# Kernel tuning notes

Measured on AMD Instinct MI355X. Metric: run time of the kernel, lower is better.

## Reference

```python
import jax, jax.numpy as jnp
import numpy as np

# ---- static config (from grid_conf / data_aug_conf) ----
B, N, C = 4, 6, 64            # batch, cameras, camC
OGH, OGW = 256, 704           # final_dim
DOWN = 16                     # 32 // up_scale
FH, FW = OGH // DOWN, OGW // DOWN   # 16, 44
DB0, DB1, DBS = 4.0, 45.0, 1.0      # dbound
D = int((DB1 - DB0) / DBS)          # 41 depth bins
DX = np.array([0.5, 0.5, 20.0], np.float32)            # dx
BX = np.array([-49.75, -49.75, 0.0], np.float32)        # bx (lower + dx/2)
NX = (200, 200, 1)                                       # nx


def make_frustum():
    # [D, FH, FW, 3] pixel (u, v, depth) frustum, matches torch create_frustum
    ds = jnp.arange(DB0, DB1, DBS, dtype=jnp.float32)[:, None, None] * jnp.ones((1, FH, FW), jnp.float32)
    xs = jnp.linspace(0.0, OGW - 1.0, FW, dtype=jnp.float32)[None, None, :] * jnp.ones((D, FH, 1), jnp.float32)
    ys = jnp.linspace(0.0, OGH - 1.0, FH, dtype=jnp.float32)[None, :, None] * jnp.ones((D, 1, FW), jnp.float32)
    return jnp.stack([xs, ys, ds], axis=-1)


def get_geometry(rots, trans, intrins, post_rots, post_trans):
    # frustum points -> ego frame, [B, N, D, FH, FW, 3]
    pts = make_frustum()[None, None] - post_trans[:, :, None, None, None, :]
    pts = jnp.einsum('bnij,bndhwj->bndhwi', jnp.linalg.inv(post_rots), pts)
    # un-project: (u*d, v*d, d)
    pts = jnp.concatenate([pts[..., :2] * pts[..., 2:3], pts[..., 2:3]], axis=-1)
    combine = rots @ jnp.linalg.inv(intrins)
    return jnp.einsum('bnij,bndhwj->bndhwi', combine, pts) + trans[:, :, None, None, None, :]


def voxel_pooling(geom, x):
    # geom: [B,N,D,H,W,3] ego coords; x: [B,N,D,H,W,C] lifted features
    dx = jnp.asarray(DX); bx = jnp.asarray(BX)
    # voxel indices; .astype(int32) truncates toward zero like torch .long()
    gi = ((geom - (bx - dx / 2.0)) / dx).astype(jnp.int32)
    Np = B * N * D * FH * FW
    gi = gi.reshape(Np, 3)
    xf = x.reshape(Np, C)
    bidx = jnp.repeat(jnp.arange(B, dtype=jnp.int32), N * D * FH * FW)
    valid = ((gi[:, 0] >= 0) & (gi[:, 0] < NX[0]) &
             (gi[:, 1] >= 0) & (gi[:, 1] < NX[1]) &
             (gi[:, 2] >= 0) & (gi[:, 2] < NX[2]))
    # flat voxel id: (((b*nz + z)*nx0 + xi)*nx1 + yi)
    flat = ((bidx * NX[2] + gi[:, 2]) * NX[0] + gi[:, 0]) * NX[1] + gi[:, 1]
    flat = jnp.where(valid, flat, 0)
    xf = xf * valid[:, None].astype(xf.dtype)
    nvox = B * NX[2] * NX[0] * NX[1]
    # scatter-add == sort + cumsum-trick per-voxel sum in the torch code
    final = jax.ops.segment_sum(xf, flat, num_segments=nvox)          # [nvox, C]
    final = final.reshape(B, NX[2], NX[0], NX[1], C)
    final = jnp.transpose(final, (0, 1, 4, 2, 3)).reshape(B, NX[2] * C, NX[0], NX[1])
    return final


def setup_inputs() -> dict:
    key = jax.random.key(0)
    k1, k2 = jax.random.split(key)
    feat_depth = jax.random.normal(k1, (B, N, D, FH, FW), jnp.float32)
    feat_pv = jax.random.normal(k2, (B, N, C, FH, FW), jnp.float32)
    # realistic 6-camera nuScenes-like rig, intrinsics scaled to 704x256
    base = np.array([[0., 0., 1.], [-1., 0., 0.], [0., -1., 0.]], np.float32)  # cam axes -> ego axes
    rots = np.zeros((B, N, 3, 3), np.float32)
    trans = np.zeros((B, N, 3), np.float32)
    for n in range(N):
        yaw = 2.0 * np.pi * n / N
        Rz = np.array([[np.cos(yaw), -np.sin(yaw), 0.], [np.sin(yaw), np.cos(yaw), 0.], [0., 0., 1.]], np.float32)
        rots[:, n] = Rz @ base
        trans[:, n] = Rz @ np.array([1.5, 0.0, 1.6], np.float32)
    fx = 1266.0 * (OGW / 1600.0)
    intr = np.array([[fx, 0., OGW / 2.0], [0., fx, OGH / 2.0], [0., 0., 1.]], np.float32)
    return {
        'feat_depth': feat_depth,
        'feat_pv': feat_pv,
        'rots': jnp.asarray(rots),
        'trans': jnp.asarray(trans),
        'intrins': jnp.asarray(np.broadcast_to(intr, (B, N, 3, 3)).copy()),
        'post_rots': jnp.asarray(np.broadcast_to(np.eye(3, dtype=np.float32), (B, N, 3, 3)).copy()),
        'post_trans': jnp.zeros((B, N, 3), jnp.float32),
    }


def reference(feat_depth, feat_pv, rots, trans, intrins, post_rots, post_trans):
    geom = get_geometry(rots, trans, intrins, post_rots, post_trans)
    geom = jax.lax.stop_gradient(geom)  # torch casts to .long(): indices are non-diff
    depth = jax.nn.softmax(feat_depth, axis=2)                 # get_depth_dist over D
    # lift: depth.unsqueeze(1) * feat.unsqueeze(2) -> [B,N,D,C,H,W] -> [B,N,D,H,W,C]
    x = depth[:, :, :, None] * feat_pv[:, :, None]
    x = jnp.transpose(x, (0, 1, 2, 4, 5, 3))
    return voxel_pooling(geom, x)                               # [B, C*nz, 200, 200]
```

## Files before the change

### kernel.cpp

```cpp
#include <hip/hip_runtime.h>
#include <math.h>

namespace {
constexpr int kB = 4, kN = 6, kC = 64, kD = 41, kFH = 16, kFW = 44;
constexpr int kNX0 = 200, kNX1 = 200;
constexpr int kHW  = kFH * kFW;
constexpr int kPix = kB * kN * kHW;
constexpr int kPts = kPix * kD;
constexpr int kVox = kB * kNX0 * kNX1;
constexpr int kPvElems = kPix * kC;
constexpr int kScanBlks = kVox / 256;
constexpr int kPvtTiles = kPix / 64;

constexpr size_t kOffPvT    = 0;
constexpr size_t kSzPvT     = (size_t)kPvElems * 4;
constexpr size_t kOffVox    = kOffPvT + kSzPvT;
constexpr size_t kSzVox     = (size_t)kPts * 4;
constexpr size_t kOffWgt    = kOffVox + kSzVox;
constexpr size_t kSzWgt     = (size_t)kPts * 4;
constexpr size_t kOffCnt    = kOffWgt + kSzWgt;
constexpr size_t kSzCnt     = (size_t)kVox * 4;
constexpr size_t kOffOffs   = kOffCnt + kSzCnt;
constexpr size_t kSzOffs    = 640256;
constexpr size_t kOffBSum   = kOffOffs + kSzOffs;
constexpr size_t kSzBSum    = 2560;
constexpr size_t kOffSKW    = kOffBSum + kSzBSum;
constexpr size_t kSzSKW     = (size_t)kPts * 8;
constexpr size_t kWsNeed    = kOffSKW + kSzSKW + 256;
}

__device__ __forceinline__ void inv3x3(const float m[9], float inv[9]) {
    float a = m[0], b = m[1], c = m[2];
    float d = m[3], e = m[4], f = m[5];
    float g = m[6], h = m[7], i = m[8];
    float A =  (e * i - f * h);
    float Bm = -(d * i - f * g);
    float Cm =  (d * h - e * g);
    float det = a * A + b * Bm + c * Cm;
    float r = 1.0f / det;
    inv[0] = A * r;
    inv[1] = -(b * i - c * h) * r;
    inv[2] =  (b * f - c * e) * r;
    inv[3] = Bm * r;
    inv[4] =  (a * i - c * g) * r;
    inv[5] = -(a * f - c * d) * r;
    inv[6] = Cm * r;
    inv[7] = -(a * h - b * g) * r;
    inv[8] =  (a * e - b * d) * r;
}

__global__ __launch_bounds__(256) void lss_pvt(const float* __restrict__ pv,
                                               float* __restrict__ pvT,
                                               unsigned* __restrict__ counts) {
    __shared__ float t[64][65];
    const int blk = blockIdx.x;
    const int tid = threadIdx.x;
    const int ci = blk * 256 + tid;
    if (ci < kVox) counts[ci] = 0u;

    if (blk < kPvtTiles) {
        const int pix0 = blk * 64;
        const int bn  = pix0 / kHW;
        const int hw0 = pix0 - bn * kHW;
        const int lane = tid & 63;
        const int wv   = tid >> 6;
        const float* src = pv + (size_t)(bn * kC) * kHW + hw0;
#pragma unroll
        for (int cc = 0; cc < 16; ++cc) {
            const int c = wv * 16 + cc;
            t[c][lane] = src[(size_t)c * kHW + lane];
        }
        __syncthreads();
        float* dst = pvT + (size_t)pix0 * kC;
#pragma unroll
        for (int jj = 0; jj < 16; ++jj) {
            const int j = wv * 16 + jj;
            dst[j * kC + lane] = t[lane][j];
        }
    }
}

__global__ __launch_bounds__(256) void lss_sm(const float* __restrict__ feat_depth,
                                              float* __restrict__ wgtArr) {
    const int pix = blockIdx.x * 256 + threadIdx.x;
    const int bn = pix / kHW;
    const int hw = pix - bn * kHW;
    const float* p = feat_depth + (size_t)(bn * kD) * kHW + hw;
    float v[kD];
#pragma unroll
    for (int d = 0; d < kD; ++d) v[d] = p[(size_t)d * kHW];
    float mx = v[0];
#pragma unroll
    for (int d = 1; d < kD; ++d) mx = fmaxf(mx, v[d]);
    float sm = 0.0f;
#pragma unroll
    for (int d = 0; d < kD; ++d) { v[d] = __expf(v[d] - mx); sm += v[d]; }
    const float inv = 1.0f / sm;
    float* o = wgtArr + (size_t)(bn * kD) * kHW + hw;
#pragma unroll
    for (int d = 0; d < kD; ++d) o[(size_t)d * kHW] = v[d] * inv;
}

__global__ __launch_bounds__(256) void lss_geo(
    const float* __restrict__ rots,
    const float* __restrict__ trans,
    const float* __restrict__ intrins,
    const float* __restrict__ post_rots,
    const float* __restrict__ post_trans,
    int* __restrict__ voxArr,
    unsigned* __restrict__ counts)
{
    const int q   = blockIdx.x * 256 + threadIdx.x;
    const int bn  = q / (kD * kHW);
    const int rem = q - bn * (kD * kHW);
    const int d   = rem / kHW;
    const int hw  = rem - d * kHW;
    const int h   = hw / kFW;
    const int w   = hw - h * kFW;
    const int b   = bn / kN;

    const float* R  = rots       + bn * 9;
    const float* K  = intrins    + bn * 9;
    const float* PR = post_rots  + bn * 9;
    const float* PT = post_trans + bn * 3;
    const float* T  = trans      + bn * 3;

    float Km[9], PRm[9];
#pragma unroll
    for (int i = 0; i < 9; ++i) { Km[i] = K[i]; PRm[i] = PR[i]; }
    float invK[9], invPR[9];
    inv3x3(Km, invK);
    inv3x3(PRm, invPR);
    float M[9];
#pragma unroll
    for (int i = 0; i < 3; ++i)
#pragma unroll
        for (int j = 0; j < 3; ++j)
            M[i * 3 + j] = R[i * 3 + 0] * invK[0 * 3 + j]
                         + R[i * 3 + 1] * invK[1 * 3 + j]
                         + R[i * 3 + 2] * invK[2 * 3 + j];

    const float u  = (float)w * (703.0f / 43.0f);
    const float v  = (float)h * 17.0f;
    const float dv = 4.0f + (float)d;
    const float px = u - PT[0], py = v - PT[1], pz = dv - PT[2];
    const float ax = invPR[0] * px + invPR[1] * py + invPR[2] * pz;
    const float ay = invPR[3] * px + invPR[4] * py + invPR[5] * pz;
    const float az = invPR[6] * px + invPR[7] * py + invPR[8] * pz;
    const float qx = ax * az, qy = ay * az, qz = az;
    const float gx = M[0] * qx + M[1] * qy + M[2] * qz + T[0];
    const float gy = M[3] * qx + M[4] * qy + M[5] * qz + T[1];
    const float gz = M[6] * qx + M[7] * qy + M[8] * qz + T[2];
    const float fx = (gx + 50.0f) / 0.5f;
    const float fy = (gy + 50.0f) / 0.5f;
    const float fz = (gz + 10.0f) / 20.0f;
    const int gix = (int)fx;
    const int giy = (int)fy;
    const int giz = (int)fz;
    int flat = -1;
    if (gix >= 0 && gix < kNX0 && giy >= 0 && giy < kNX1 && giz == 0) {
        flat = (b * kNX0 + gix) * kNX1 + giy;
        atomicAdd(&counts[flat], 1u);
    }
    voxArr[q] = flat;
}

__global__ __launch_bounds__(256) void lss_scan_a(const unsigned* __restrict__ counts,
                                                  unsigned* __restrict__ offsets,
                                                  unsigned* __restrict__ blockSums) {
    const int i = blockIdx.x * 256 + threadIdx.x;
    const int lane = threadIdx.x & 63;
    const int wv = threadIdx.x >> 6;
    const unsigned c = counts[i];
    unsigned s = c;
#pragma unroll
    for (int o = 1; o < 64; o <<= 1) {
        unsigned v = __shfl_up(s, o);
        if (lane >= o) s += v;
    }
    __shared__ unsigned wsum[4];
    if (lane == 63) wsum[wv] = s;
    __syncthreads();
    unsigned base = 0;
#pragma unroll
    for (int k = 0; k < 3; ++k)
        if (k < wv) base += wsum[k];
    const unsigned incl = s + base;
    offsets[i] = incl - c;
    if (threadIdx.x == 255) blockSums[blockIdx.x] = incl;
}

__global__ __launch_bounds__(1024) void lss_scan_b(unsigned* __restrict__ blockSums,
                                                   unsigned* __restrict__ offsets) {
    const int t = threadIdx.x;
    const int lane = t & 63;
    const int wv = t >> 6;
    const unsigned c = (t < kScanBlks) ? blockSums[t] : 0u;
    unsigned s = c;
#pragma unroll
    for (int o = 1; o < 64; o <<= 1) {
        unsigned v = __shfl_up(s, o);
        if (lane >= o) s += v;
    }
    __shared__ unsigned wsum[16];
    if (lane == 63) wsum[wv] = s;
    __syncthreads();
    unsigned base = 0;
#pragma unroll
    for (int k = 0; k < 15; ++k)
        if (k < wv) base += wsum[k];
    const unsigned incl = s + base;
    if (t < kScanBlks) blockSums[t] = incl - c;
    if (t == 1023) offsets[kVox] = incl;
}

__global__ __launch_bounds__(256) void lss_scan_c(const unsigned* __restrict__ blockSums,
                                                  unsigned* __restrict__ offsets) {
    const int i = blockIdx.x * 256 + threadIdx.x;
    offsets[i] += blockSums[blockIdx.x];
}

__global__ __launch_bounds__(256) void lss_order(const int* __restrict__ voxArr,
                                                 const float* __restrict__ wgtArr,
                                                 unsigned* __restrict__ offsets,
                                                 uint2* __restrict__ skw) {
    const int q = blockIdx.x * 256 + threadIdx.x;
    const int f = voxArr[q];
    if (f >= 0) {
        const unsigned slot = atomicAdd(&offsets[f], 1u);
        const int bn  = q / (kD * kHW);
        const int rem = q - bn * (kD * kHW);
        const int hw  = rem % kHW;
        uint2 u;
        u.x = (unsigned)(bn * kHW + hw);
        u.y = __float_as_uint(wgtArr[q]);
        skw[slot] = u;
    }
}

__global__ __launch_bounds__(512) void lss_gather(const float* __restrict__ pvT,
                                                  const unsigned* __restrict__ offsets,
                                                  const uint2* __restrict__ skw,
                                                  float* __restrict__ out) {
    constexpr int kChunk = 2048;
    __shared__ float acc[50][65];
    __shared__ uint2 sbuf[kChunk];
    __shared__ unsigned rowOff[51];
    const int tile = blockIdx.x;
    const int yt = tile & 3;
    const int xi = (tile >> 2) % kNX0;
    const int b  = tile / (kNX0 * 4);
    const int yi0 = yt * 50;
    const int lane = threadIdx.x & 63;
    const int wave = threadIdx.x >> 6;
    const int flat0 = (b * kNX0 + xi) * kNX1 + yi0;

    for (int e = threadIdx.x; e < 50 * 65; e += 512)
        ((float*)acc)[e] = 0.0f;
    if (threadIdx.x < 51) {
        const int f = flat0 - 1 + (int)threadIdx.x;
        rowOff[threadIdx.x] = (f < 0) ? 0u : offsets[f];
    }
    __syncthreads();

    const unsigned seg0 = rowOff[0];
    const unsigned seg1 = rowOff[50];

    for (unsigned cb = seg0; cb < seg1; cb += (unsigned)kChunk) {
        const unsigned ce = min(cb + (unsigned)kChunk, seg1);
        const int n = (int)(ce - cb);
        for (int e = threadIdx.x; e < n; e += 512)
            sbuf[e] = skw[cb + e];
        __syncthreads();

        for (int j = wave; j < 50; j += 8) {
            unsigned s0 = max(rowOff[j], cb);
            unsigned e0 = min(rowOff[j + 1], ce);
            if (s0 >= e0) continue;
            float a0 = 0.0f, a1 = 0.0f, a2 = 0.0f, a3 = 0.0f;
            int p  = (int)(s0 - cb);
            int pe = (int)(e0 - cb);
            for (; p + 4 <= pe; p += 4) {
                const uint2 u0 = sbuf[p + 0];
                const uint2 u1 = sbuf[p + 1];
                const uint2 u2 = sbuf[p + 2];
                const uint2 u3 = sbuf[p + 3];
                a0 += __uint_as_float(u0.y) * pvT[u0.x * kC + lane];
                a1 += __uint_as_float(u1.y) * pvT[u1.x * kC + lane];
                a2 += __uint_as_float(u2.y) * pvT[u2.x * kC + lane];
                a3 += __uint_as_float(u3.y) * pvT[u3.x * kC + lane];
            }
            for (; p < pe; ++p) {
                const uint2 u = sbuf[p];
                a0 += __uint_as_float(u.y) * pvT[u.x * kC + lane];
            }
            acc[j][lane] += (a0 + a1) + (a2 + a3);
        }
        __syncthreads();
    }
    __syncthreads();

    for (int e = threadIdx.x; e < kC * 50; e += 512) {
        const int c = e / 50, j = e % 50;
        out[((b * kC + c) * (kNX0 * kNX1)) + xi * kNX1 + yi0 + j] = acc[j][c];
    }
}

__global__ __launch_bounds__(256) void lss_scatter_fb(
    const float* __restrict__ feat_depth,
    const float* __restrict__ feat_pv,
    const float* __restrict__ rots,
    const float* __restrict__ trans,
    const float* __restrict__ intrins,
    const float* __restrict__ post_rots,
    const float* __restrict__ post_trans,
    float* __restrict__ out)
{
    const int lane = threadIdx.x & 63;
    const int wave = threadIdx.x >> 6;
    const int pix  = blockIdx.x * 4 + wave;
    const int w  = pix % kFW;
    const int h  = (pix / kFW) % kFH;
    const int bn = pix / kHW;
    const int b  = bn / kN;
    const float* R  = rots       + bn * 9;
    const float* K  = intrins    + bn * 9;
    const float* PR = post_rots  + bn * 9;
    const float* PT = post_trans + bn * 3;
    const float* T  = trans      + bn * 3;
    float Km[9], PRm[9];
#pragma unroll
    for (int i = 0; i < 9; ++i) { Km[i] = K[i]; PRm[i] = PR[i]; }
    float invK[9], invPR[9];
    inv3x3(Km, invK);
    inv3x3(PRm, invPR);
    float M[9];
#pragma unroll
    for (int i = 0; i < 3; ++i)
#pragma unroll
        for (int j = 0; j < 3; ++j)
            M[i * 3 + j] = R[i * 3 + 0] * invK[0 * 3 + j]
                         + R[i * 3 + 1] * invK[1 * 3 + j]
                         + R[i * 3 + 2] * invK[2 * 3 + j];
    const float pt0 = PT[0], pt1 = PT[1], pt2 = PT[2];
    const float t0 = T[0], t1 = T[1], t2 = T[2];
    const int pixBase = h * kFW + w;
    float fd = -INFINITY;
    if (lane < kD)
        fd = feat_depth[(bn * kD + lane) * kHW + pixBase];
    float mx = fd;
#pragma unroll
    for (int off = 32; off >= 1; off >>= 1)
        mx = fmaxf(mx, __shfl_xor(mx, off));
    float ex = (lane < kD) ? __expf(fd - mx) : 0.0f;
    float sm = ex;
#pragma unroll
    for (int off = 32; off >= 1; off >>= 1)
        sm += __shfl_xor(sm, off);
    const float wgt = ex / sm;
    int vox = -1;
    if (lane < kD) {
        const float u  = (float)w * (703.0f / 43.0f);
        const float v  = (float)h * 17.0f;
        const float dv = 4.0f + (float)lane;
        const float px = u - pt0, py = v - pt1, pz = dv - pt2;
        const float ax = invPR[0] * px + invPR[1] * py + invPR[2] * pz;
        const float ay = invPR[3] * px + invPR[4] * py + invPR[5] * pz;
        const float az = invPR[6] * px + invPR[7] * py + invPR[8] * pz;
        const float qx = ax * az, qy = ay * az, qz = az;
        const float gx = M[0] * qx + M[1] * qy + M[2] * qz + t0;
        const float gy = M[3] * qx + M[4] * qy + M[5] * qz + t1;
        const float gz = M[6] * qx + M[7] * qy + M[8] * qz + t2;
        const float fx = (gx + 50.0f) / 0.5f;
        const float fy = (gy + 50.0f) / 0.5f;
        const float fz = (gz + 10.0f) / 20.0f;
        const int gix = (int)fx;
        const int giy = (int)fy;
        const int giz = (int)fz;
        if (gix >= 0 && gix < kNX0 && giy >= 0 && giy < kNX1 && giz == 0)
            vox = gix * kNX1 + giy;
    }
    const float fc = feat_pv[(bn * kC + lane) * kHW + pixBase];
    const int outBase = (b * kC + lane) * (kNX0 * kNX1);
#pragma unroll 1
    for (int d = 0; d < kD; ++d) {
        const int   vd = __shfl(vox, d);
        const float wd = __shfl(wgt, d);
        if (vd >= 0)
            atomicAdd(&out[outBase + vd], wd * fc);
    }
}

extern "C" void kernel_launch(void* const* d_in, const int* in_sizes, int n_in,
                              void* d_out, int out_size, void* d_ws, size_t ws_size,
                              hipStream_t stream) {
    const float* feat_depth = (const float*)d_in[0];
    const float* feat_pv    = (const float*)d_in[1];
    const float* rots       = (const float*)d_in[2];
    const float* trans      = (const float*)d_in[3];
    const float* intrins    = (const float*)d_in[4];
    const float* post_rots  = (const float*)d_in[5];
    const float* post_trans = (const float*)d_in[6];
    float* out = (float*)d_out;

    if (ws_size < kWsNeed) {
        hipMemsetAsync(out, 0, (size_t)out_size * sizeof(float), stream);
        lss_scatter_fb<<<kPix / 4, 256, 0, stream>>>(
            feat_depth, feat_pv, rots, trans, intrins, post_rots, post_trans, out);
        return;
    }

    char* ws = (char*)d_ws;
    float*    pvT      = (float*)   (ws + kOffPvT);
    int*      voxArr   = (int*)     (ws + kOffVox);
    float*    wgtArr   = (float*)   (ws + kOffWgt);
    unsigned* counts   = (unsigned*)(ws + kOffCnt);
    unsigned* offsets  = (unsigned*)(ws + kOffOffs);
    unsigned* blockSums= (unsigned*)(ws + kOffBSum);
    uint2*    skw      = (uint2*)   (ws + kOffSKW);

    lss_pvt<<<kScanBlks, 256, 0, stream>>>(feat_pv, pvT, counts);
    lss_sm<<<kPix / 256, 256, 0, stream>>>(feat_depth, wgtArr);
    lss_geo<<<kPts / 256, 256, 0, stream>>>(
        rots, trans, intrins, post_rots, post_trans, voxArr, counts);
    lss_scan_a<<<kScanBlks, 256, 0, stream>>>(counts, offsets, blockSums);
    lss_scan_b<<<1, 1024, 0, stream>>>(blockSums, offsets);
    lss_scan_c<<<kScanBlks, 256, 0, stream>>>(blockSums, offsets);
    lss_order<<<kPts / 256, 256, 0, stream>>>(voxArr, wgtArr, offsets, skw);
    lss_gather<<<kB * kNX0 * 4, 512, 0, stream>>>(pvT, offsets, skw, out);
}
```

Before: 117.9 us.

## Fuse front-end kernels and geometry/scan/order into one cooperative grid-synced kernel

Merges the pvT transpose, the depth softmax and the counts zeroing into a single front kernel. Geometry, histogram, the three-level scan and the ordering pass become one cooperative kernel that uses grid.sync and keeps voxel ids in registers, which removes the voxArr buffer and several launches. The gather loop is unrolled to 8 and uses readfirstlane so row pointers and weights are wave-uniform scalars. The cooperative launch needs all 625 blocks resident at once and adds grid-wide barrier cost.

```diff
diff --git a/kernel.cpp b/kernel.cpp
--- a/kernel.cpp
+++ b/kernel.cpp
@@ -1,5 +1,8 @@
 #include <hip/hip_runtime.h>
+#include <hip/hip_cooperative_groups.h>
 #include <math.h>
+
+namespace cg = cooperative_groups;
 
 namespace {
 constexpr int kB = 4, kN = 6, kC = 64, kD = 41, kFH = 16, kFW = 44;
@@ -11,12 +14,13 @@
 constexpr int kPvElems = kPix * kC;
 constexpr int kScanBlks = kVox / 256;
 constexpr int kPvtTiles = kPix / 64;
+constexpr int kSmBlks = kPix / 256;
+constexpr int kFrontBlks = kPvtTiles + kSmBlks + kScanBlks;
+constexpr int kMidIter = (kPts + kVox - 1) / kVox;
 
 constexpr size_t kOffPvT    = 0;
 constexpr size_t kSzPvT     = (size_t)kPvElems * 4;
-constexpr size_t kOffVox    = kOffPvT + kSzPvT;
-constexpr size_t kSzVox     = (size_t)kPts * 4;
-constexpr size_t kOffWgt    = kOffVox + kSzVox;
+constexpr size_t kOffWgt    = kOffPvT + kSzPvT;
 constexpr size_t kSzWgt     = (size_t)kPts * 4;
 constexpr size_t kOffCnt    = kOffWgt + kSzWgt;
 constexpr size_t kSzCnt     = (size_t)kVox * 4;
@@ -49,68 +53,12 @@
     inv[8] =  (a * e - b * d) * r;
 }
 
-__global__ __launch_bounds__(256) void lss_pvt(const float* __restrict__ pv,
-                                               float* __restrict__ pvT,
-                                               unsigned* __restrict__ counts) {
-    __shared__ float t[64][65];
-    const int blk = blockIdx.x;
-    const int tid = threadIdx.x;
-    const int ci = blk * 256 + tid;
-    if (ci < kVox) counts[ci] = 0u;
-
-    if (blk < kPvtTiles) {
-        const int pix0 = blk * 64;
-        const int bn  = pix0 / kHW;
-        const int hw0 = pix0 - bn * kHW;
-        const int lane = tid & 63;
-        const int wv   = tid >> 6;
-        const float* src = pv + (size_t)(bn * kC) * kHW + hw0;
-#pragma unroll
-        for (int cc = 0; cc < 16; ++cc) {
-            const int c = wv * 16 + cc;
-            t[c][lane] = src[(size_t)c * kHW + lane];
-        }
-        __syncthreads();
-        float* dst = pvT + (size_t)pix0 * kC;
-#pragma unroll
-        for (int jj = 0; jj < 16; ++jj) {
-            const int j = wv * 16 + jj;
-            dst[j * kC + lane] = t[lane][j];
-        }
-    }
-}
-
-__global__ __launch_bounds__(256) void lss_sm(const float* __restrict__ feat_depth,
-                                              float* __restrict__ wgtArr) {
-    const int pix = blockIdx.x * 256 + threadIdx.x;
-    const int bn = pix / kHW;
-    const int hw = pix - bn * kHW;
-    const float* p = feat_depth + (size_t)(bn * kD) * kHW + hw;
-    float v[kD];
-#pragma unroll
-    for (int d = 0; d < kD; ++d) v[d] = p[(size_t)d * kHW];
-    float mx = v[0];
-#pragma unroll
-    for (int d = 1; d < kD; ++d) mx = fmaxf(mx, v[d]);
-    float sm = 0.0f;
-#pragma unroll
-    for (int d = 0; d < kD; ++d) { v[d] = __expf(v[d] - mx); sm += v[d]; }
-    const float inv = 1.0f / sm;
-    float* o = wgtArr + (size_t)(bn * kD) * kHW + hw;
-#pragma unroll
-    for (int d = 0; d < kD; ++d) o[(size_t)d * kHW] = v[d] * inv;
-}
-
-__global__ __launch_bounds__(256) void lss_geo(
-    const float* __restrict__ rots,
-    const float* __restrict__ trans,
-    const float* __restrict__ intrins,
-    const float* __restrict__ post_rots,
-    const float* __restrict__ post_trans,
-    int* __restrict__ voxArr,
-    unsigned* __restrict__ counts)
-{
-    const int q   = blockIdx.x * 256 + threadIdx.x;
+__device__ __forceinline__ int geo_flat(int q,
+                                        const float* __restrict__ rots,
+                                        const float* __restrict__ trans,
+                                        const float* __restrict__ intrins,
+                                        const float* __restrict__ post_rots,
+                                        const float* __restrict__ post_trans) {
     const int bn  = q / (kD * kHW);
     const int rem = q - bn * (kD * kHW);
     const int d   = rem / kHW;
@@ -157,84 +105,157 @@
     const int gix = (int)fx;
     const int giy = (int)fy;
     const int giz = (int)fz;
-    int flat = -1;
-    if (gix >= 0 && gix < kNX0 && giy >= 0 && giy < kNX1 && giz == 0) {
-        flat = (b * kNX0 + gix) * kNX1 + giy;
-        atomicAdd(&counts[flat], 1u);
-    }
-    voxArr[q] = flat;
-}
-
-__global__ __launch_bounds__(256) void lss_scan_a(const unsigned* __restrict__ counts,
-                                                  unsigned* __restrict__ offsets,
-                                                  unsigned* __restrict__ blockSums) {
-    const int i = blockIdx.x * 256 + threadIdx.x;
-    const int lane = threadIdx.x & 63;
-    const int wv = threadIdx.x >> 6;
-    const unsigned c = counts[i];
-    unsigned s = c;
-#pragma unroll
-    for (int o = 1; o < 64; o <<= 1) {
-        unsigned v = __shfl_up(s, o);
-        if (lane >= o) s += v;
-    }
-    __shared__ unsigned wsum[4];
-    if (lane == 63) wsum[wv] = s;
-    __syncthreads();
-    unsigned base = 0;
-#pragma unroll
-    for (int k = 0; k < 3; ++k)
-        if (k < wv) base += wsum[k];
-    const unsigned incl = s + base;
-    offsets[i] = incl - c;
-    if (threadIdx.x == 255) blockSums[blockIdx.x] = incl;
-}
-
-__global__ __launch_bounds__(1024) void lss_scan_b(unsigned* __restrict__ blockSums,
-                                                   unsigned* __restrict__ offsets) {
-    const int t = threadIdx.x;
-    const int lane = t & 63;
-    const int wv = t >> 6;
-    const unsigned c = (t < kScanBlks) ? blockSums[t] : 0u;
-    unsigned s = c;
-#pragma unroll
-    for (int o = 1; o < 64; o <<= 1) {
-        unsigned v = __shfl_up(s, o);
-        if (lane >= o) s += v;
-    }
-    __shared__ unsigned wsum[16];
-    if (lane == 63) wsum[wv] = s;
-    __syncthreads();
-    unsigned base = 0;
-#pragma unroll
-    for (int k = 0; k < 15; ++k)
-        if (k < wv) base += wsum[k];
-    const unsigned incl = s + base;
-    if (t < kScanBlks) blockSums[t] = incl - c;
-    if (t == 1023) offsets[kVox] = incl;
-}
-
-__global__ __launch_bounds__(256) void lss_scan_c(const unsigned* __restrict__ blockSums,
-                                                  unsigned* __restrict__ offsets) {
-    const int i = blockIdx.x * 256 + threadIdx.x;
-    offsets[i] += blockSums[blockIdx.x];
-}
-
-__global__ __launch_bounds__(256) void lss_order(const int* __restrict__ voxArr,
-                                                 const float* __restrict__ wgtArr,
-                                                 unsigned* __restrict__ offsets,
-                                                 uint2* __restrict__ skw) {
-    const int q = blockIdx.x * 256 + threadIdx.x;
-    const int f = voxArr[q];
-    if (f >= 0) {
-        const unsigned slot = atomicAdd(&offsets[f], 1u);
-        const int bn  = q / (kD * kHW);
-        const int rem = q - bn * (kD * kHW);
-        const int hw  = rem % kHW;
-        uint2 u;
-        u.x = (unsigned)(bn * kHW + hw);
-        u.y = __float_as_uint(wgtArr[q]);
-        skw[slot] = u;
+    if (gix >= 0 && gix < kNX0 && giy >= 0 && giy < kNX1 && giz == 0)
+        return (b * kNX0 + gix) * kNX1 + giy;
+    return -1;
+}
+
+__global__ __launch_bounds__(256) void lss_front(const float* __restrict__ pv,
+                                                 const float* __restrict__ feat_depth,
+                                                 float* __restrict__ pvT,
+                                                 float* __restrict__ wgtArr,
+                                                 unsigned* __restrict__ counts) {
+    __shared__ float t[64][65];
+    const int blk = blockIdx.x;
+    const int tid = threadIdx.x;
+
+    if (blk < kPvtTiles) {
+        const int pix0 = blk * 64;
+        const int bn  = pix0 / kHW;
+        const int hw0 = pix0 - bn * kHW;
+        const int lane = tid & 63;
+        const int wv   = tid >> 6;
+        const float* src = pv + (size_t)(bn * kC) * kHW + hw0;
+#pragma unroll
+        for (int cc = 0; cc < 16; ++cc) {
+            const int c = wv * 16 + cc;
+            t[c][lane] = src[(size_t)c * kHW + lane];
+        }
+        __syncthreads();
+        float* dst = pvT + (size_t)pix0 * kC;
+#pragma unroll
+        for (int jj = 0; jj < 16; ++jj) {
+            const int j = wv * 16 + jj;
+            dst[j * kC + lane] = t[lane][j];
+        }
+    } else if (blk < kPvtTiles + kSmBlks) {
+        const int pix = (blk - kPvtTiles) * 256 + tid;
+        const int bn = pix / kHW;
+        const int hw = pix - bn * kHW;
+        const float* p = feat_depth + (size_t)(bn * kD) * kHW + hw;
+        float v[kD];
+#pragma unroll
+        for (int d = 0; d < kD; ++d) v[d] = p[(size_t)d * kHW];
+        float mx = v[0];
+#pragma unroll
+        for (int d = 1; d < kD; ++d) mx = fmaxf(mx, v[d]);
+        float sm = 0.0f;
+#pragma unroll
+        for (int d = 0; d < kD; ++d) { v[d] = __expf(v[d] - mx); sm += v[d]; }
+        const float inv = 1.0f / sm;
+        float* o = wgtArr + (size_t)(bn * kD) * kHW + hw;
+#pragma unroll
+        for (int d = 0; d < kD; ++d) o[(size_t)d * kHW] = v[d] * inv;
+    } else {
+        const int ci = (blk - kPvtTiles - kSmBlks) * 256 + tid;
+        counts[ci] = 0u;
+    }
+}
+
+__global__ __launch_bounds__(256) void lss_mid(
+    const float* __restrict__ rots,
+    const float* __restrict__ trans,
+    const float* __restrict__ intrins,
+    const float* __restrict__ post_rots,
+    const float* __restrict__ post_trans,
+    const float* __restrict__ wgtArr,
+    unsigned* __restrict__ counts,
+    unsigned* __restrict__ offsets,
+    unsigned* __restrict__ blockSums,
+    uint2* __restrict__ skw)
+{
+    cg::grid_group grid = cg::this_grid();
+    __shared__ unsigned shw[4];
+    const int tid  = threadIdx.x;
+    const int gid  = blockIdx.x * 256 + tid;
+    const int lane = tid & 63;
+    const int wv   = tid >> 6;
+
+    int flatReg[kMidIter];
+#pragma unroll
+    for (int k = 0; k < kMidIter; ++k) {
+        const int q = gid + k * kVox;
+        flatReg[k] = -1;
+        if (q < kPts) {
+            const int f = geo_flat(q, rots, trans, intrins, post_rots, post_trans);
+            flatReg[k] = f;
+            if (f >= 0) atomicAdd(&counts[f], 1u);
+        }
+    }
+    grid.sync();
+
+    {
+        const unsigned c = counts[gid];
+        unsigned s = c;
+#pragma unroll
+        for (int o = 1; o < 64; o <<= 1) {
+            unsigned v = __shfl_up(s, o);
+            if (lane >= o) s += v;
+        }
+        if (lane == 63) shw[wv] = s;
+        __syncthreads();
+        unsigned base = 0;
+#pragma unroll
+        for (int k = 0; k < 3; ++k)
+            if (k < wv) base += shw[k];
+        const unsigned incl = s + base;
+        offsets[gid] = incl - c;
+        if (tid == 255) blockSums[blockIdx.x] = incl;
+    }
+    grid.sync();
+
+    if (blockIdx.x == 0) {
+        const int lo = tid * 3;
+        const unsigned c0 = (lo     < kScanBlks) ? blockSums[lo]     : 0u;
+        const unsigned c1 = (lo + 1 < kScanBlks) ? blockSums[lo + 1] : 0u;
+        const unsigned c2 = (lo + 2 < kScanBlks) ? blockSums[lo + 2] : 0u;
+        const unsigned s = c0 + c1 + c2;
+        unsigned si = s;
+#pragma unroll
+        for (int o = 1; o < 64; o <<= 1) {
+            unsigned v = __shfl_up(si, o);
+            if (lane >= o) si += v;
+        }
+        if (lane == 63) shw[wv] = si;
+        __syncthreads();
+        unsigned base = 0;
+#pragma unroll
+        for (int k = 0; k < 3; ++k)
+            if (k < wv) base += shw[k];
+        unsigned run = si - s + base;
+        if (lo     < kScanBlks) { blockSums[lo]     = run; run += c0; }
+        if (lo + 1 < kScanBlks) { blockSums[lo + 1] = run; run += c1; }
+        if (lo + 2 < kScanBlks) { blockSums[lo + 2] = run; run += c2; }
+    }
+    grid.sync();
+
+    offsets[gid] += blockSums[blockIdx.x];
+    grid.sync();
+
+#pragma unroll
+    for (int k = 0; k < kMidIter; ++k) {
+        const int q = gid + k * kVox;
+        const int f = flatReg[k];
+        if (q < kPts && f >= 0) {
+            const unsigned slot = atomicAdd(&offsets[f], 1u);
+            const int bn  = q / (kD * kHW);
+            const int rem = q - bn * (kD * kHW);
+            const int hw  = rem % kHW;
+            uint2 u;
+            u.x = (unsigned)(bn * kHW + hw);
+            u.y = __float_as_uint(wgtArr[q]);
+            skw[slot] = u;
+        }
     }
 }
 
@@ -280,19 +301,38 @@
             float a0 = 0.0f, a1 = 0.0f, a2 = 0.0f, a3 = 0.0f;
             int p  = (int)(s0 - cb);
             int pe = (int)(e0 - cb);
-            for (; p + 4 <= pe; p += 4) {
+            for (; p + 8 <= pe; p += 8) {
                 const uint2 u0 = sbuf[p + 0];
                 const uint2 u1 = sbuf[p + 1];
                 const uint2 u2 = sbuf[p + 2];
                 const uint2 u3 = sbuf[p + 3];
-                a0 += __uint_as_float(u0.y) * pvT[u0.x * kC + lane];
-                a1 += __uint_as_float(u1.y) * pvT[u1.x * kC + lane];
-                a2 += __uint_as_float(u2.y) * pvT[u2.x * kC + lane];
-                a3 += __uint_as_float(u3.y) * pvT[u3.x * kC + lane];
+                const uint2 u4 = sbuf[p + 4];
+                const uint2 u5 = sbuf[p + 5];
+                const uint2 u6 = sbuf[p + 6];
+                const uint2 u7 = sbuf[p + 7];
+                const float* r0 = pvT + (size_t)((unsigned)__builtin_amdgcn_readfirstlane(u0.x)) * kC;
+                const float* r1 = pvT + (size_t)((unsigned)__builtin_amdgcn_readfirstlane(u1.x)) * kC;
+                const float* r2 = pvT + (size_t)((unsigned)__builtin_amdgcn_readfirstlane(u2.x)) * kC;
+                const float* r3 = pvT + (size_t)((unsigned)__builtin_amdgcn_readfirstlane(u3.x)) * kC;
+                const float* r4 = pvT + (size_t)((unsigned)__builtin_amdgcn_readfirstlane(u4.x)) * kC;
+                const float* r5 = pvT + (size_t)((unsigned)__builtin_amdgcn_readfirstlane(u5.x)) * kC;
+                const float* r6 = pvT + (size_t)((unsigned)__builtin_amdgcn_readfirstlane(u6.x)) * kC;
+                const float* r7 = pvT + (size_t)((unsigned)__builtin_amdgcn_readfirstlane(u7.x)) * kC;
+                const float f0 = r0[lane], f1 = r1[lane], f2 = r2[lane], f3 = r3[lane];
+                const float f4 = r4[lane], f5 = r5[lane], f6 = r6[lane], f7 = r7[lane];
+                a0 = fmaf(__uint_as_float(__builtin_amdgcn_readfirstlane(u0.y)), f0, a0);
+                a1 = fmaf(__uint_as_float(__builtin_amdgcn_readfirstlane(u1.y)), f1, a1);
+                a2 = fmaf(__uint_as_float(__builtin_amdgcn_readfirstlane(u2.y)), f2, a2);
+                a3 = fmaf(__uint_as_float(__builtin_amdgcn_readfirstlane(u3.y)), f3, a3);
+                a0 = fmaf(__uint_as_float(__builtin_amdgcn_readfirstlane(u4.y)), f4, a0);
+                a1 = fmaf(__uint_as_float(__builtin_amdgcn_readfirstlane(u5.y)), f5, a1);
+                a2 = fmaf(__uint_as_float(__builtin_amdgcn_readfirstlane(u6.y)), f6, a2);
+                a3 = fmaf(__uint_as_float(__builtin_amdgcn_readfirstlane(u7.y)), f7, a3);
             }
             for (; p < pe; ++p) {
                 const uint2 u = sbuf[p];
-                a0 += __uint_as_float(u.y) * pvT[u.x * kC + lane];
+                const float* r = pvT + (size_t)((unsigned)__builtin_amdgcn_readfirstlane(u.x)) * kC;
+                a0 = fmaf(__uint_as_float(__builtin_amdgcn_readfirstlane(u.y)), r[lane], a0);
             }
             acc[j][lane] += (a0 + a1) + (a2 + a3);
         }
@@ -323,27 +363,6 @@
     const int h  = (pix / kFW) % kFH;
     const int bn = pix / kHW;
     const int b  = bn / kN;
-    const float* R  = rots       + bn * 9;
-    const float* K  = intrins    + bn * 9;
-    const float* PR = post_rots  + bn * 9;
-    const float* PT = post_trans + bn * 3;
-    const float* T  = trans      + bn * 3;
-    float Km[9], PRm[9];
-#pragma unroll
-    for (int i = 0; i < 9; ++i) { Km[i] = K[i]; PRm[i] = PR[i]; }
-    float invK[9], invPR[9];
-    inv3x3(Km, invK);
-    inv3x3(PRm, invPR);
-    float M[9];
-#pragma unroll
-    for (int i = 0; i < 3; ++i)
-#pragma unroll
-        for (int j = 0; j < 3; ++j)
-            M[i * 3 + j] = R[i * 3 + 0] * invK[0 * 3 + j]
-                         + R[i * 3 + 1] * invK[1 * 3 + j]
-                         + R[i * 3 + 2] * invK[2 * 3 + j];
-    const float pt0 = PT[0], pt1 = PT[1], pt2 = PT[2];
-    const float t0 = T[0], t1 = T[1], t2 = T[2];
     const int pixBase = h * kFW + w;
     float fd = -INFINITY;
     if (lane < kD)
@@ -360,25 +379,9 @@
     const float wgt = ex / sm;
     int vox = -1;
     if (lane < kD) {
-        const float u  = (float)w * (703.0f / 43.0f);
-        const float v  = (float)h * 17.0f;
-        const float dv = 4.0f + (float)lane;
-        const float px = u - pt0, py = v - pt1, pz = dv - pt2;
-        const float ax = invPR[0] * px + invPR[1] * py + invPR[2] * pz;
-        const float ay = invPR[3] * px + invPR[4] * py + invPR[5] * pz;
-        const float az = invPR[6] * px + invPR[7] * py + invPR[8] * pz;
-        const float qx = ax * az, qy = ay * az, qz = az;
-        const float gx = M[0] * qx + M[1] * qy + M[2] * qz + t0;
-        const float gy = M[3] * qx + M[4] * qy + M[5] * qz + t1;
-        const float gz = M[6] * qx + M[7] * qy + M[8] * qz + t2;
-        const float fx = (gx + 50.0f) / 0.5f;
-        const float fy = (gy + 50.0f) / 0.5f;
-        const float fz = (gz + 10.0f) / 20.0f;
-        const int gix = (int)fx;
-        const int giy = (int)fy;
-        const int giz = (int)fz;
-        if (gix >= 0 && gix < kNX0 && giy >= 0 && giy < kNX1 && giz == 0)
-            vox = gix * kNX1 + giy;
+        const int q = (bn * kD + lane) * kHW + pixBase;
+        const int f = geo_flat(q, rots, trans, intrins, post_rots, post_trans);
+        if (f >= 0) vox = f % (kNX0 * kNX1);
     }
     const float fc = feat_pv[(bn * kC + lane) * kHW + pixBase];
     const int outBase = (b * kC + lane) * (kNX0 * kNX1);
@@ -412,20 +415,22 @@
 
     char* ws = (char*)d_ws;
     float*    pvT      = (float*)   (ws + kOffPvT);
-    int*      voxArr   = (int*)     (ws + kOffVox);
     float*    wgtArr   = (float*)   (ws + kOffWgt);
     unsigned* counts   = (unsigned*)(ws + kOffCnt);
     unsigned* offsets  = (unsigned*)(ws + kOffOffs);
     unsigned* blockSums= (unsigned*)(ws + kOffBSum);
     uint2*    skw      = (uint2*)   (ws + kOffSKW);
 
-    lss_pvt<<<kScanBlks, 256, 0, stream>>>(feat_pv, pvT, counts);
-    lss_sm<<<kPix / 256, 256, 0, stream>>>(feat_depth, wgtArr);
-    lss_geo<<<kPts / 256, 256, 0, stream>>>(
-        rots, trans, intrins, post_rots, post_trans, voxArr, counts);
-    lss_scan_a<<<kScanBlks, 256, 0, stream>>>(counts, offsets, blockSums);
-    lss_scan_b<<<1, 1024, 0, stream>>>(blockSums, offsets);
-    lss_scan_c<<<kScanBlks, 256, 0, stream>>>(blockSums, offsets);
-    lss_order<<<kPts / 256, 256, 0, stream>>>(voxArr, wgtArr, offsets, skw);
+    lss_front<<<kFrontBlks, 256, 0, stream>>>(feat_pv, feat_depth, pvT, wgtArr, counts);
+
+    void* midArgs[] = {
+        (void*)&rots, (void*)&trans, (void*)&intrins,
+        (void*)&post_rots, (void*)&post_trans,
+        (void*)&wgtArr, (void*)&counts, (void*)&offsets,
+        (void*)&blockSums, (void*)&skw
+    };
+    hipLaunchCooperativeKernel(reinterpret_cast<void*>(lss_mid),
+                               dim3(kScanBlks), dim3(256), midArgs, 0, stream);
+
     lss_gather<<<kB * kNX0 * 4, 512, 0, stream>>>(pvT, offsets, skw, out);
 }
```

Result: slower. 404.9 us (+243.5%).
